# Kernel tuning notes

Hardware: AMD Instinct MI355X
Metric: run time of the kernel (lower is better)

The kernel has to match this reference:

```python
import jax, jax.numpy as jnp
import numpy as np

N_SRC = 50000
N_DST = 50000
N_EDGES = 1600000
BATCH = 64


def setup_inputs() -> dict:
    key = jax.random.key(0)
    k1, k2, k3, k4, k5 = jax.random.split(key, 5)
    x = jax.random.normal(k1, (BATCH, N_SRC), dtype=jnp.float32)
    # per-edge scalar weights, init like Synapse.init_weight: U(-v, v), v = sqrt(1/fan_in)~sqrt(1/32)
    v = float(np.sqrt(1.0 / 32.0))
    k = jax.random.uniform(k2, (N_EDGES,), dtype=jnp.float32, minval=-v, maxval=v)
    b = jax.random.normal(k3, (N_DST,), dtype=jnp.float32) * 0.1
    edge_src = jax.random.randint(k4, (N_EDGES,), 0, N_SRC, dtype=jnp.int32)
    edge_dst = jax.random.randint(k5, (N_EDGES,), 0, N_DST, dtype=jnp.int32)
    return {"x": x, "k": k, "b": b, "edge_src": edge_src, "edge_dst": edge_dst}


def reference(x, k, b, edge_src, edge_dst):
    # Synapse: out_e = k_e * source_output  (source output is x[:, src(e)], shape [batch])
    # msgs: [n_edges, batch]
    msgs = x.T[edge_src] * k[:, None]
    # DestinationNeuron: sum of dendrite outputs per destination + bias
    agg = jax.ops.segment_sum(msgs, edge_dst, num_segments=N_DST)  # [n_dst, batch]
    out = jax.nn.relu(agg.T + b[None, :])  # [batch, n_dst]
    return out
```

## Files before the change

### kernel.cpp

```cpp
#include <hip/hip_runtime.h>
#include <hip/hip_bf16.h>
#include <stdint.h>

#define N_SRC 50000
#define N_DST 50000
#define N_EDGES 1600000
#define BATCH 64

#define DPB 32
#define NBUCK ((N_DST + DPB - 1) / DPB)
#define CAPB 1344
#define EPB 6400
#define PTHREADS 1024
#define GTHREADS 512

__global__ void transpose_kernel(const float* __restrict__ x,
                                 __hip_bfloat16* __restrict__ xTb,
                                 int* __restrict__ gcur) {
    __shared__ float tile[64][65];
    const int s0 = blockIdx.x * 64;
    const int tid = threadIdx.x;

    if (gcur && tid < 2) {
        const int i = blockIdx.x * 2 + tid;
        if (i < NBUCK) gcur[i] = 0;
    }

#pragma unroll
    for (int it = 0; it < 16; ++it) {
        const int i = it * 256 + tid;
        const int bi = i >> 6;
        const int sc = i & 63;
        const int s = s0 + sc;
        float v = 0.0f;
        if (s < N_SRC) v = x[(size_t)bi * N_SRC + s];
        tile[bi][sc] = v;
    }
    __syncthreads();
#pragma unroll
    for (int it = 0; it < 16; ++it) {
        const int i = it * 256 + tid;
        const int sc = i >> 6;
        const int bi = i & 63;
        const int s = s0 + sc;
        if (s < N_SRC) xTb[(size_t)s * 64 + bi] = __float2bfloat16(tile[bi][sc]);
    }
}

__global__ __launch_bounds__(PTHREADS) void partition_kernel(
        const float* __restrict__ k,
        const int* __restrict__ esrc,
        const int* __restrict__ edst,
        int* __restrict__ gcur,
        uint64_t* __restrict__ part) {
    __shared__ int bcnt[NBUCK];
    __shared__ int bcur[NBUCK];
    const int e0 = blockIdx.x * EPB;
    const int n = min(EPB, N_EDGES - e0);

    for (int i = threadIdx.x; i < NBUCK; i += PTHREADS) bcnt[i] = 0;
    __syncthreads();
    for (int i = threadIdx.x; i < n; i += PTHREADS)
        atomicAdd(&bcnt[edst[e0 + i] >> 5], 1);
    __syncthreads();
    for (int bi = threadIdx.x; bi < NBUCK; bi += PTHREADS) {
        const int c = bcnt[bi];
        bcur[bi] = c ? atomicAdd(&gcur[bi], c) : 0;
    }
    __syncthreads();
    for (int i = threadIdx.x; i < n; i += PTHREADS) {
        const int e = e0 + i;
        const int d = edst[e];
        const int bkt = d >> 5;
        const int slot = atomicAdd(&bcur[bkt], 1);
        if (slot < CAPB) {
            const uint32_t lo = (uint32_t)esrc[e] | ((uint32_t)(d & 31) << 16);
            part[(size_t)bkt * CAPB + slot] =
                (uint64_t)lo | ((uint64_t)__float_as_uint(k[e]) << 32);
        }
    }
}

__global__ __launch_bounds__(GTHREADS, 8) void gather_kernel(
        const __hip_bfloat16* __restrict__ xTb,
        const int* __restrict__ gcur,
        const uint64_t* __restrict__ part,
        const float* __restrict__ b,
        float* __restrict__ out) {
    __shared__ uint64_t raw[CAPB];
    __shared__ uint64_t sorted[CAPB];
    __shared__ int dbase[DPB + 1];
    __shared__ int dcur[DPB];

    const uint32_t* __restrict__ xTu = (const uint32_t*)xTb;

    const int bk = blockIdx.x;
    const size_t base = (size_t)bk * CAPB;
    const int n = min(gcur[bk], CAPB);
    const int d0 = bk * DPB;
    const int tid = threadIdx.x;
    const int wid = tid >> 6;
    const int lane = tid & 63;
    const int h = lane >> 5;
    const int m = lane & 31;

    if (tid < DPB) dcur[tid] = 0;
    __syncthreads();

    for (int i = tid; i < n; i += GTHREADS) {
        const uint64_t r = part[base + i];
        raw[i] = r;
        atomicAdd(&dcur[(int)((r >> 16) & 31)], 1);
    }
    __syncthreads();

    if (wid == 0) {
        const int orig = (lane < DPB) ? dcur[lane] : 0;
        int v = orig;
#pragma unroll
        for (int d = 1; d < DPB; d <<= 1) {
            const int t = __shfl_up(v, d, 64);
            if (lane >= d) v += t;
        }
        if (lane < DPB) dbase[lane] = v - orig;
        if (lane == DPB - 1) dbase[DPB] = v;
    }
    __syncthreads();
    if (tid < DPB) dcur[tid] = dbase[tid];
    __syncthreads();

    for (int i = tid; i < n; i += GTHREADS) {
        const uint64_t r = raw[i];
        const int p = atomicAdd(&dcur[(int)((r >> 16) & 31)], 1);
        sorted[p] = r;
    }
    __syncthreads();

    float ax[4], ay[4];
    const int dlo = wid * 4;
#pragma unroll
    for (int q = 0; q < 4; ++q) {
        const int dl = dlo + q;
        const int d = d0 + dl;
        float px = 0.0f, py = 0.0f;
        if (d < N_DST) {
            int j = dbase[dl];
            const int je = dbase[dl + 1];
            for (; j + 8 <= je; j += 8) {
                const uint64_t r0 = sorted[j + 0 + h];
                const uint64_t r1 = sorted[j + 2 + h];
                const uint64_t r2 = sorted[j + 4 + h];
                const uint64_t r3 = sorted[j + 6 + h];
                const uint32_t x0 = xTu[(size_t)((uint32_t)r0 & 0xFFFFu) * 32 + m];
                const uint32_t x1 = xTu[(size_t)((uint32_t)r1 & 0xFFFFu) * 32 + m];
                const uint32_t x2 = xTu[(size_t)((uint32_t)r2 & 0xFFFFu) * 32 + m];
                const uint32_t x3 = xTu[(size_t)((uint32_t)r3 & 0xFFFFu) * 32 + m];
                const float k0 = __uint_as_float((uint32_t)(r0 >> 32));
                const float k1 = __uint_as_float((uint32_t)(r1 >> 32));
                const float k2 = __uint_as_float((uint32_t)(r2 >> 32));
                const float k3 = __uint_as_float((uint32_t)(r3 >> 32));
                px = fmaf(k0, __uint_as_float(x0 << 16), px);
                py = fmaf(k0, __uint_as_float(x0 & 0xFFFF0000u), py);
                px = fmaf(k1, __uint_as_float(x1 << 16), px);
                py = fmaf(k1, __uint_as_float(x1 & 0xFFFF0000u), py);
                px = fmaf(k2, __uint_as_float(x2 << 16), px);
                py = fmaf(k2, __uint_as_float(x2 & 0xFFFF0000u), py);
                px = fmaf(k3, __uint_as_float(x3 << 16), px);
                py = fmaf(k3, __uint_as_float(x3 & 0xFFFF0000u), py);
            }
            for (; j < je; j += 2) {
                const int idx = j + h;
                const bool v = idx < je;
                const uint64_t r = sorted[v ? idx : j];
                const float kv = v ? __uint_as_float((uint32_t)(r >> 32)) : 0.0f;
                const uint32_t xv = xTu[(size_t)((uint32_t)r & 0xFFFFu) * 32 + m];
                px = fmaf(kv, __uint_as_float(xv << 16), px);
                py = fmaf(kv, __uint_as_float(xv & 0xFFFF0000u), py);
            }
        }
        px += __shfl_xor(px, 32);
        py += __shfl_xor(py, 32);
        ax[q] = px;
        ay[q] = py;
    }
    __syncthreads();

    float* stg = (float*)sorted;
    if (h == 0) {
#pragma unroll
        for (int q = 0; q < 4; ++q) {
            const int dl = dlo + q;
            stg[dl * 65 + 2 * m]     = ax[q];
            stg[dl * 65 + 2 * m + 1] = ay[q];
        }
    }
    __syncthreads();

    for (int i = tid; i < 64 * DPB; i += GTHREADS) {
        const int dl = i & (DPB - 1);
        const int bi = i >> 5;
        const int d = d0 + dl;
        if (d < N_DST)
            out[(size_t)bi * N_DST + d] = fmaxf(stg[dl * 65 + bi] + b[d], 0.0f);
    }
}

__global__ void scatter_kernel(const __hip_bfloat16* __restrict__ xTb,
                               const float* __restrict__ k,
                               const int* __restrict__ esrc,
                               const int* __restrict__ edst,
                               float* __restrict__ agg) {
    const int gtid = blockIdx.x * blockDim.x + threadIdx.x;
    const int wid = gtid >> 6;
    const int lane = threadIdx.x & 63;
    const int nwaves = (gridDim.x * blockDim.x) >> 6;
    for (int e = wid; e < N_EDGES; e += nwaves) {
        atomicAdd(&agg[(size_t)edst[e] * 64 + lane],
                  k[e] * __bfloat162float(xTb[(size_t)esrc[e] * 64 + lane]));
    }
}

__global__ void finish_kernel(const float* __restrict__ agg,
                              const float* __restrict__ b,
                              float* __restrict__ out) {
    __shared__ float tile[64 * 65];
    const int d0 = blockIdx.x * 64;
    const int tid = threadIdx.x;
#pragma unroll
    for (int it = 0; it < 16; ++it) {
        const int i = it * 256 + tid;
        const int dl = i >> 6;
        const int bi = i & 63;
        const int d = d0 + dl;
        float v = 0.0f;
        if (d < N_DST) v = agg[(size_t)d * 64 + bi];
        tile[bi * 65 + dl] = v;
    }
    __syncthreads();
#pragma unroll
    for (int it = 0; it < 16; ++it) {
        const int i = it * 256 + tid;
        const int bi = i >> 6;
        const int dl = i & 63;
        const int d = d0 + dl;
        if (d < N_DST)
            out[(size_t)bi * N_DST + d] = fmaxf(tile[bi * 65 + dl] + b[d], 0.0f);
    }
}

extern "C" void kernel_launch(void* const* d_in, const int* in_sizes, int n_in,
                              void* d_out, int out_size, void* d_ws, size_t ws_size,
                              hipStream_t stream) {
    const float* x    = (const float*)d_in[0];
    const float* k    = (const float*)d_in[1];
    const float* b    = (const float*)d_in[2];
    const int*   esrc = (const int*)d_in[3];
    const int*   edst = (const int*)d_in[4];
    float* out = (float*)d_out;

    const size_t xt_bytes   = (size_t)N_SRC * 64 * sizeof(__hip_bfloat16);
    const size_t part_bytes = (size_t)NBUCK * CAPB * sizeof(uint64_t);
    const size_t off_gcur   = xt_bytes + part_bytes;
    const size_t need_new   = off_gcur + ((NBUCK * 4 + 4095) & ~4095ull);

    __hip_bfloat16* xTb = (__hip_bfloat16*)d_ws;
    const int nblk_t = (N_SRC + 63) / 64;

    if (ws_size >= need_new) {
        uint64_t* part = (uint64_t*)((char*)d_ws + xt_bytes);
        int* gcur      = (int*)((char*)d_ws + off_gcur);

        transpose_kernel<<<nblk_t, 256, 0, stream>>>(x, xTb, gcur);
        const int nblk_p = (N_EDGES + EPB - 1) / EPB;
        partition_kernel<<<nblk_p, PTHREADS, 0, stream>>>(k, esrc, edst,
                                                          gcur, part);
        gather_kernel<<<NBUCK, GTHREADS, 0, stream>>>(xTb, gcur, part, b, out);
    } else {
        transpose_kernel<<<nblk_t, 256, 0, stream>>>(x, xTb, nullptr);
        float* agg = (float*)((char*)d_ws + ((xt_bytes + 255) & ~255ull));
        hipMemsetAsync(agg, 0, (size_t)N_DST * 64 * sizeof(float), stream);
        scatter_kernel<<<2048, 256, 0, stream>>>(xTb, k, esrc, edst, agg);
        const int nblk_f = (N_DST + 63) / 64;
        finish_kernel<<<nblk_f, 256, 0, stream>>>(agg, b, out);
    }
}
```

Measured before the change: 73.83 us.

## Split transposed bf16 source table into two batch-half planes for gather

The transposed bf16 x table now has two planes, each holding 32 batch entries per source row (64 bytes), instead of one 128-byte row. The gather kernel makes two passes, one per batch half, with 16 lanes per edge and 4 edges per wave instruction. The aim is to shrink each plane's working set so gathered rows stay resident in cache. The cost is re-reading the sorted edge list twice and extra shuffle reductions. The fallback scatter path is adapted to the same layout.

Result: slower. 82.37 us (+11.6%).

```diff
diff --git a/kernel.cpp b/kernel.cpp
--- a/kernel.cpp
+++ b/kernel.cpp
@@ -15,7 +15,7 @@
 #define GTHREADS 512
 
 __global__ void transpose_kernel(const float* __restrict__ x,
-                                 __hip_bfloat16* __restrict__ xTb,
+                                 uint32_t* __restrict__ xTh,
                                  int* __restrict__ gcur) {
     __shared__ float tile[64][65];
     const int s0 = blockIdx.x * 64;
@@ -38,12 +38,18 @@
     }
     __syncthreads();
 #pragma unroll
-    for (int it = 0; it < 16; ++it) {
-        const int i = it * 256 + tid;
-        const int sc = i >> 6;
-        const int bi = i & 63;
+    for (int it = 0; it < 8; ++it) {
+        const int i = it * 256 + tid;
+        const int sc = i >> 5;
+        const int p = i & 31;
         const int s = s0 + sc;
-        if (s < N_SRC) xTb[(size_t)s * 64 + bi] = __float2bfloat16(tile[bi][sc]);
+        if (s < N_SRC) {
+            __hip_bfloat16 b0 = __float2bfloat16(tile[2 * p][sc]);
+            __hip_bfloat16 b1 = __float2bfloat16(tile[2 * p + 1][sc]);
+            const uint32_t val = (uint32_t)*(uint16_t*)&b0 |
+                                 ((uint32_t)*(uint16_t*)&b1 << 16);
+            xTh[((size_t)(p >> 4) * N_SRC + s) * 16 + (p & 15)] = val;
+        }
     }
 }
 
@@ -82,7 +88,7 @@
 }
 
 __global__ __launch_bounds__(GTHREADS, 8) void gather_kernel(
-        const __hip_bfloat16* __restrict__ xTb,
+        const uint32_t* __restrict__ xTh,
         const int* __restrict__ gcur,
         const uint64_t* __restrict__ part,
         const float* __restrict__ b,
@@ -92,8 +98,6 @@
     __shared__ int dbase[DPB + 1];
     __shared__ int dcur[DPB];
 
-    const uint32_t* __restrict__ xTu = (const uint32_t*)xTb;
-
     const int bk = blockIdx.x;
     const size_t base = (size_t)bk * CAPB;
     const int n = min(gcur[bk], CAPB);
@@ -101,8 +105,8 @@
     const int tid = threadIdx.x;
     const int wid = tid >> 6;
     const int lane = tid & 63;
-    const int h = lane >> 5;
-    const int m = lane & 31;
+    const int rp = lane >> 4;
+    const int m = lane & 15;
 
     if (tid < DPB) dcur[tid] = 0;
     __syncthreads();
@@ -136,63 +140,58 @@
     }
     __syncthreads();
 
-    float ax[4], ay[4];
+    float acc[2][4][2];
     const int dlo = wid * 4;
 #pragma unroll
-    for (int q = 0; q < 4; ++q) {
-        const int dl = dlo + q;
-        const int d = d0 + dl;
-        float px = 0.0f, py = 0.0f;
-        if (d < N_DST) {
+    for (int bh = 0; bh < 2; ++bh) {
+        const uint32_t* __restrict__ xh = xTh + (size_t)bh * N_SRC * 16;
+#pragma unroll
+        for (int q = 0; q < 4; ++q) {
+            const int dl = dlo + q;
+            float px = 0.0f, py = 0.0f;
             int j = dbase[dl];
             const int je = dbase[dl + 1];
             for (; j + 8 <= je; j += 8) {
-                const uint64_t r0 = sorted[j + 0 + h];
-                const uint64_t r1 = sorted[j + 2 + h];
-                const uint64_t r2 = sorted[j + 4 + h];
-                const uint64_t r3 = sorted[j + 6 + h];
-                const uint32_t x0 = xTu[(size_t)((uint32_t)r0 & 0xFFFFu) * 32 + m];
-                const uint32_t x1 = xTu[(size_t)((uint32_t)r1 & 0xFFFFu) * 32 + m];
-                const uint32_t x2 = xTu[(size_t)((uint32_t)r2 & 0xFFFFu) * 32 + m];
-                const uint32_t x3 = xTu[(size_t)((uint32_t)r3 & 0xFFFFu) * 32 + m];
+                const uint64_t r0 = sorted[j + rp];
+                const uint64_t r1 = sorted[j + 4 + rp];
+                const uint32_t x0 = xh[(size_t)((uint32_t)r0 & 0xFFFFu) * 16 + m];
+                const uint32_t x1 = xh[(size_t)((uint32_t)r1 & 0xFFFFu) * 16 + m];
                 const float k0 = __uint_as_float((uint32_t)(r0 >> 32));
                 const float k1 = __uint_as_float((uint32_t)(r1 >> 32));
-                const float k2 = __uint_as_float((uint32_t)(r2 >> 32));
-                const float k3 = __uint_as_float((uint32_t)(r3 >> 32));
                 px = fmaf(k0, __uint_as_float(x0 << 16), px);
                 py = fmaf(k0, __uint_as_float(x0 & 0xFFFF0000u), py);
                 px = fmaf(k1, __uint_as_float(x1 << 16), px);
                 py = fmaf(k1, __uint_as_float(x1 & 0xFFFF0000u), py);
-                px = fmaf(k2, __uint_as_float(x2 << 16), px);
-                py = fmaf(k2, __uint_as_float(x2 & 0xFFFF0000u), py);
-                px = fmaf(k3, __uint_as_float(x3 << 16), px);
-                py = fmaf(k3, __uint_as_float(x3 & 0xFFFF0000u), py);
             }
-            for (; j < je; j += 2) {
-                const int idx = j + h;
+            for (; j < je; j += 4) {
+                const int idx = j + rp;
                 const bool v = idx < je;
                 const uint64_t r = sorted[v ? idx : j];
                 const float kv = v ? __uint_as_float((uint32_t)(r >> 32)) : 0.0f;
-                const uint32_t xv = xTu[(size_t)((uint32_t)r & 0xFFFFu) * 32 + m];
+                const uint32_t xv = xh[(size_t)((uint32_t)r & 0xFFFFu) * 16 + m];
                 px = fmaf(kv, __uint_as_float(xv << 16), px);
                 py = fmaf(kv, __uint_as_float(xv & 0xFFFF0000u), py);
             }
-        }
-        px += __shfl_xor(px, 32);
-        py += __shfl_xor(py, 32);
-        ax[q] = px;
-        ay[q] = py;
+            px += __shfl_xor(px, 16);
+            px += __shfl_xor(px, 32);
+            py += __shfl_xor(py, 16);
+            py += __shfl_xor(py, 32);
+            acc[bh][q][0] = px;
+            acc[bh][q][1] = py;
+        }
     }
     __syncthreads();
 
     float* stg = (float*)sorted;
-    if (h == 0) {
-#pragma unroll
-        for (int q = 0; q < 4; ++q) {
-            const int dl = dlo + q;
-            stg[dl * 65 + 2 * m]     = ax[q];
-            stg[dl * 65 + 2 * m + 1] = ay[q];
-        }
+    if (rp == 0) {
+#pragma unroll
+        for (int bh = 0; bh < 2; ++bh)
+#pragma unroll
+            for (int q = 0; q < 4; ++q) {
+                const int dl = dlo + q;
+                stg[dl * 65 + bh * 32 + 2 * m]     = acc[bh][q][0];
+                stg[dl * 65 + bh * 32 + 2 * m + 1] = acc[bh][q][1];
+            }
     }
     __syncthreads();
 
@@ -205,7 +204,7 @@
     }
 }
 
-__global__ void scatter_kernel(const __hip_bfloat16* __restrict__ xTb,
+__global__ void scatter_kernel(const uint32_t* __restrict__ xTh,
                                const float* __restrict__ k,
                                const int* __restrict__ esrc,
                                const int* __restrict__ edst,
@@ -214,9 +213,11 @@
     const int wid = gtid >> 6;
     const int lane = threadIdx.x & 63;
     const int nwaves = (gridDim.x * blockDim.x) >> 6;
+    const int bh = lane >> 5, m = (lane >> 1) & 15, hi = lane & 1;
     for (int e = wid; e < N_EDGES; e += nwaves) {
-        atomicAdd(&agg[(size_t)edst[e] * 64 + lane],
-                  k[e] * __bfloat162float(xTb[(size_t)esrc[e] * 64 + lane]));
+        const uint32_t xv = xTh[((size_t)bh * N_SRC + esrc[e]) * 16 + m];
+        const float xf = __uint_as_float(hi ? (xv & 0xFFFF0000u) : (xv << 16));
+        atomicAdd(&agg[(size_t)edst[e] * 64 + lane], k[e] * xf);
     }
 }
 
@@ -258,28 +259,28 @@
     const int*   edst = (const int*)d_in[4];
     float* out = (float*)d_out;
 
-    const size_t xt_bytes   = (size_t)N_SRC * 64 * sizeof(__hip_bfloat16);
+    const size_t xt_bytes   = (size_t)2 * N_SRC * 16 * sizeof(uint32_t);
     const size_t part_bytes = (size_t)NBUCK * CAPB * sizeof(uint64_t);
     const size_t off_gcur   = xt_bytes + part_bytes;
     const size_t need_new   = off_gcur + ((NBUCK * 4 + 4095) & ~4095ull);
 
-    __hip_bfloat16* xTb = (__hip_bfloat16*)d_ws;
+    uint32_t* xTh = (uint32_t*)d_ws;
     const int nblk_t = (N_SRC + 63) / 64;
 
     if (ws_size >= need_new) {
         uint64_t* part = (uint64_t*)((char*)d_ws + xt_bytes);
         int* gcur      = (int*)((char*)d_ws + off_gcur);
 
-        transpose_kernel<<<nblk_t, 256, 0, stream>>>(x, xTb, gcur);
+        transpose_kernel<<<nblk_t, 256, 0, stream>>>(x, xTh, gcur);
         const int nblk_p = (N_EDGES + EPB - 1) / EPB;
         partition_kernel<<<nblk_p, PTHREADS, 0, stream>>>(k, esrc, edst,
                                                           gcur, part);
-        gather_kernel<<<NBUCK, GTHREADS, 0, stream>>>(xTb, gcur, part, b, out);
+        gather_kernel<<<NBUCK, GTHREADS, 0, stream>>>(xTh, gcur, part, b, out);
     } else {
-        transpose_kernel<<<nblk_t, 256, 0, stream>>>(x, xTb, nullptr);
+        transpose_kernel<<<nblk_t, 256, 0, stream>>>(x, xTh, nullptr);
         float* agg = (float*)((char*)d_ws + ((xt_bytes + 255) & ~255ull));
         hipMemsetAsync(agg, 0, (size_t)N_DST * 64 * sizeof(float), stream);
-        scatter_kernel<<<2048, 256, 0, stream>>>(xTb, k, esrc, edst, agg);
+        scatter_kernel<<<2048, 256, 0, stream>>>(xTh, k, esrc, edst, agg);
         const int nblk_f = (N_DST + 63) / 64;
         finish_kernel<<<nblk_f, 256, 0, stream>>>(agg, b, out);
     }
```

## Gather with 8-byte bf16 loads, four edges per wavefront step; halve partition EPB

Applied to the files above, without the earlier changes.

The gather loop now has each 16-lane group load a uint2 holding four bf16 batch values, so one wavefront covers four edges per step instead of two. Partial sums are reduced with two xor shuffles. The goal is fewer, wider global load instructions per edge and more edges in flight per wave. Separately, edges-per-block in the partition kernel is halved to 3200, which launches more partition blocks. The trade-off is one extra shuffle round, more partition blocks, and the removal of the d<N_DST guard, which relies on empty buckets past the last destination.

Result: slower. 80.25 us (+8.7%).

```diff
diff --git a/kernel.cpp b/kernel.cpp
--- a/kernel.cpp
+++ b/kernel.cpp
@@ -10,7 +10,7 @@
 #define DPB 32
 #define NBUCK ((N_DST + DPB - 1) / DPB)
 #define CAPB 1344
-#define EPB 6400
+#define EPB 3200
 #define PTHREADS 1024
 #define GTHREADS 512
 
@@ -92,7 +92,7 @@
     __shared__ int dbase[DPB + 1];
     __shared__ int dcur[DPB];
 
-    const uint32_t* __restrict__ xTu = (const uint32_t*)xTb;
+    const uint2* __restrict__ xTu2 = (const uint2*)xTb;
 
     const int bk = blockIdx.x;
     const size_t base = (size_t)bk * CAPB;
@@ -101,8 +101,8 @@
     const int tid = threadIdx.x;
     const int wid = tid >> 6;
     const int lane = tid & 63;
-    const int h = lane >> 5;
-    const int m = lane & 31;
+    const int rp = lane >> 4;
+    const int m = lane & 15;
 
     if (tid < DPB) dcur[tid] = 0;
     __syncthreads();
@@ -136,62 +136,58 @@
     }
     __syncthreads();
 
-    float ax[4], ay[4];
+    float acc[4][4];
     const int dlo = wid * 4;
 #pragma unroll
     for (int q = 0; q < 4; ++q) {
         const int dl = dlo + q;
-        const int d = d0 + dl;
-        float px = 0.0f, py = 0.0f;
-        if (d < N_DST) {
-            int j = dbase[dl];
-            const int je = dbase[dl + 1];
-            for (; j + 8 <= je; j += 8) {
-                const uint64_t r0 = sorted[j + 0 + h];
-                const uint64_t r1 = sorted[j + 2 + h];
-                const uint64_t r2 = sorted[j + 4 + h];
-                const uint64_t r3 = sorted[j + 6 + h];
-                const uint32_t x0 = xTu[(size_t)((uint32_t)r0 & 0xFFFFu) * 32 + m];
-                const uint32_t x1 = xTu[(size_t)((uint32_t)r1 & 0xFFFFu) * 32 + m];
-                const uint32_t x2 = xTu[(size_t)((uint32_t)r2 & 0xFFFFu) * 32 + m];
-                const uint32_t x3 = xTu[(size_t)((uint32_t)r3 & 0xFFFFu) * 32 + m];
-                const float k0 = __uint_as_float((uint32_t)(r0 >> 32));
-                const float k1 = __uint_as_float((uint32_t)(r1 >> 32));
-                const float k2 = __uint_as_float((uint32_t)(r2 >> 32));
-                const float k3 = __uint_as_float((uint32_t)(r3 >> 32));
-                px = fmaf(k0, __uint_as_float(x0 << 16), px);
-                py = fmaf(k0, __uint_as_float(x0 & 0xFFFF0000u), py);
-                px = fmaf(k1, __uint_as_float(x1 << 16), px);
-                py = fmaf(k1, __uint_as_float(x1 & 0xFFFF0000u), py);
-                px = fmaf(k2, __uint_as_float(x2 << 16), px);
-                py = fmaf(k2, __uint_as_float(x2 & 0xFFFF0000u), py);
-                px = fmaf(k3, __uint_as_float(x3 << 16), px);
-                py = fmaf(k3, __uint_as_float(x3 & 0xFFFF0000u), py);
-            }
-            for (; j < je; j += 2) {
-                const int idx = j + h;
-                const bool v = idx < je;
-                const uint64_t r = sorted[v ? idx : j];
-                const float kv = v ? __uint_as_float((uint32_t)(r >> 32)) : 0.0f;
-                const uint32_t xv = xTu[(size_t)((uint32_t)r & 0xFFFFu) * 32 + m];
-                px = fmaf(kv, __uint_as_float(xv << 16), px);
-                py = fmaf(kv, __uint_as_float(xv & 0xFFFF0000u), py);
-            }
-        }
-        px += __shfl_xor(px, 32);
-        py += __shfl_xor(py, 32);
-        ax[q] = px;
-        ay[q] = py;
+        float a0 = 0.0f, a1 = 0.0f, a2 = 0.0f, a3 = 0.0f;
+        int j = dbase[dl];
+        const int je = dbase[dl + 1];
+        for (; j + 8 <= je; j += 8) {
+            const uint64_t r0 = sorted[j + rp];
+            const uint64_t r1 = sorted[j + 4 + rp];
+            const uint2 x0 = xTu2[(size_t)((uint32_t)r0 & 0xFFFFu) * 16 + m];
+            const uint2 x1 = xTu2[(size_t)((uint32_t)r1 & 0xFFFFu) * 16 + m];
+            const float k0 = __uint_as_float((uint32_t)(r0 >> 32));
+            const float k1 = __uint_as_float((uint32_t)(r1 >> 32));
+            a0 = fmaf(k0, __uint_as_float(x0.x << 16), a0);
+            a1 = fmaf(k0, __uint_as_float(x0.x & 0xFFFF0000u), a1);
+            a2 = fmaf(k0, __uint_as_float(x0.y << 16), a2);
+            a3 = fmaf(k0, __uint_as_float(x0.y & 0xFFFF0000u), a3);
+            a0 = fmaf(k1, __uint_as_float(x1.x << 16), a0);
+            a1 = fmaf(k1, __uint_as_float(x1.x & 0xFFFF0000u), a1);
+            a2 = fmaf(k1, __uint_as_float(x1.y << 16), a2);
+            a3 = fmaf(k1, __uint_as_float(x1.y & 0xFFFF0000u), a3);
+        }
+        for (; j < je; j += 4) {
+            const int idx = j + rp;
+            const bool v = idx < je;
+            const uint64_t r = sorted[v ? idx : j];
+            const float kv = v ? __uint_as_float((uint32_t)(r >> 32)) : 0.0f;
+            const uint2 xv = xTu2[(size_t)((uint32_t)r & 0xFFFFu) * 16 + m];
+            a0 = fmaf(kv, __uint_as_float(xv.x << 16), a0);
+            a1 = fmaf(kv, __uint_as_float(xv.x & 0xFFFF0000u), a1);
+            a2 = fmaf(kv, __uint_as_float(xv.y << 16), a2);
+            a3 = fmaf(kv, __uint_as_float(xv.y & 0xFFFF0000u), a3);
+        }
+        a0 += __shfl_xor(a0, 16); a0 += __shfl_xor(a0, 32);
+        a1 += __shfl_xor(a1, 16); a1 += __shfl_xor(a1, 32);
+        a2 += __shfl_xor(a2, 16); a2 += __shfl_xor(a2, 32);
+        a3 += __shfl_xor(a3, 16); a3 += __shfl_xor(a3, 32);
+        acc[q][0] = a0; acc[q][1] = a1; acc[q][2] = a2; acc[q][3] = a3;
     }
     __syncthreads();
 
     float* stg = (float*)sorted;
-    if (h == 0) {
+    if (rp == 0) {
 #pragma unroll
         for (int q = 0; q < 4; ++q) {
             const int dl = dlo + q;
-            stg[dl * 65 + 2 * m]     = ax[q];
-            stg[dl * 65 + 2 * m + 1] = ay[q];
+            stg[dl * 65 + 4 * m + 0] = acc[q][0];
+            stg[dl * 65 + 4 * m + 1] = acc[q][1];
+            stg[dl * 65 + 4 * m + 2] = acc[q][2];
+            stg[dl * 65 + 4 * m + 3] = acc[q][3];
         }
     }
     __syncthreads();
```
